# Kernel optimization log

Measured on AMD Instinct MI355X. Metric: run time of the kernel, lower is better.

Reference implementation:

```python
import jax, jax.numpy as jnp
import numpy as np

B, C, H, W = 8, 256, 32, 32
DK, HEADS = 64, 4
DQ = DK * HEADS            # lambda attention: query dim = dim_key * num_heads
DV = 256 // HEADS          # out_channels // num_heads
EPS = 1e-5
SF = DK ** (-0.25)


def setup_inputs() -> dict:
    key = jax.random.key(0)
    ks = jax.random.split(key, 6)
    inv = 1.0 / np.sqrt(C)
    return {
        "input": jax.random.normal(ks[0], (B, C, H, W), jnp.float32),
        "Wq": jax.random.normal(ks[1], (DQ, C), jnp.float32) * inv,
        "gamma_q": jnp.ones((DQ,), jnp.float32),
        "beta_q": jnp.zeros((DQ,), jnp.float32),
        "Wk": jax.random.normal(ks[2], (DK, C), jnp.float32) * inv,
        "gamma_k": jnp.ones((DK,), jnp.float32),
        "beta_k": jnp.zeros((DK,), jnp.float32),
        "Wv": jax.random.normal(ks[3], (DV, C), jnp.float32) * inv,
        "rpe": jax.random.normal(ks[4], (2 * max(H, W) - 1, 2 * max(H, W) - 1, DK), jnp.float32),
    }


def _bn(x, gamma, beta):
    # BatchNorm2d in training mode: batch stats over (B, H, W), biased variance
    mu = jnp.mean(x, axis=(0, 2, 3), keepdims=True)
    var = jnp.var(x, axis=(0, 2, 3), keepdims=True)
    xn = (x - mu) * jax.lax.rsqrt(var + EPS)
    return xn * gamma[None, :, None, None] + beta[None, :, None, None]


def reference(input, Wq, gamma_q, beta_q, Wk, gamma_k, beta_k, Wv, rpe):
    b, c, h, w = input.shape
    n = h * w
    size = max(h, w)

    # conv1x1 projections (no bias)
    q = _bn(jnp.einsum('oc,bchw->bohw', Wq, input), gamma_q, beta_q)
    k = _bn(jnp.einsum('oc,bchw->bohw', Wk, input), gamma_k, beta_k)
    v = jnp.einsum('oc,bchw->bohw', Wv, input)

    q = q.reshape(b, HEADS, DK, n) * SF          # [b,h,k,n]
    k = k.reshape(b, DK, n) * SF                 # single kv head -> [b,k,n]
    v = v.reshape(b, DV, n)                      # [b,v,n]

    # lambda attention: content lambda
    ks = jax.nn.softmax(k, axis=-1)
    context = jnp.einsum('bkn,bvn->bkv', ks, v)
    out = jnp.einsum('bkv,bhkn->bhvn', context, q)

    # positional lambda via relative position embedding gather
    pos = jnp.arange(size)
    grid = jnp.stack(jnp.meshgrid(pos, pos, indexing='ij'), axis=-1).reshape(-1, 2)  # [n,2]
    rel = grid[None, :] - grid[:, None] + (size - 1)                                 # [n,n,2]
    rg = rpe[rel[..., 0], rel[..., 1]]                                               # [n,n,k]
    pos_context = jnp.einsum('nmk,bvm->bnkv', rg, v)
    out = out + jnp.einsum('bhkn,bnkv->bhvn', q, pos_context)

    return out.reshape(b, -1, h, w)
```

## Files before the change

kernel.cpp:

```cpp
#include <hip/hip_runtime.h>

#define SFC 0.35355339059327373f

typedef __attribute__((ext_vector_type(8))) short short8;
typedef __attribute__((ext_vector_type(16))) float f32x16;
typedef unsigned short ushort_t;

__device__ __forceinline__ float4 ld4(const float* p) { return *reinterpret_cast<const float4*>(p); }
__device__ __forceinline__ void st4(float* p, float4 v) { *reinterpret_cast<float4*>(p) = v; }

union F4 { float4 v; float f[4]; };
union S8 { short8 v; ushort_t u[8]; };

__device__ __forceinline__ ushort_t bfb(float f) {
  union { float f; unsigned u; } a; a.f = f;
  unsigned r = a.u + 0x7FFFu + ((a.u >> 16) & 1u);
  return (ushort_t)(r >> 16);
}
__device__ __forceinline__ float bf2f(ushort_t u) {
  union { unsigned u; float f; } a; a.u = (unsigned)u << 16; return a.f;
}

__device__ __forceinline__ void gl16(const void* g, void* l) {
  __builtin_amdgcn_global_load_lds(
      (const __attribute__((address_space(1))) unsigned int*)g,
      (__attribute__((address_space(3))) unsigned int*)l, 16, 0, 0);
}

__global__ __launch_bounds__(256) void k_prep(
    const float* __restrict__ rpe, const float* __restrict__ wq,
    const float* __restrict__ wk, const float* __restrict__ wv,
    const float* __restrict__ x, ushort_t* __restrict__ RPEB2,
    ushort_t* __restrict__ WB, ushort_t* __restrict__ XBT)
{
  const int bx = blockIdx.x, t = threadIdx.x;
  if (bx < 63) {
    const int di = bx;
#pragma unroll
    for (int it = 0; it < 2; ++it) {
      const int slot = t + it * 256;
      const int tkc = slot >> 6;
      const int l = slot & 63, lnp = l & 31, hip = l >> 5;
      const int dj = (tkc >> 2) * 32 + lnp;
      const int k = (tkc & 3) * 16 + hip * 8;
      S8 o;
      if (dj < 63) {
        const float* s = rpe + (size_t)di * 4032 + dj * 64 + k;
        float4 a = ld4(s), b = ld4(s + 4);
        o.u[0] = bfb(a.x); o.u[1] = bfb(a.y); o.u[2] = bfb(a.z); o.u[3] = bfb(a.w);
        o.u[4] = bfb(b.x); o.u[5] = bfb(b.y); o.u[6] = bfb(b.z); o.u[7] = bfb(b.w);
      } else {
#pragma unroll
        for (int i = 0; i < 8; ++i) o.u[i] = 0;
      }
      *(short8*)(RPEB2 + (size_t)di * 4096 + tkc * 512 + l * 8) = o.v;
    }
  } else if (bx < 111) {
    const int cc = (bx - 63) * 256 + t;
    const int o = cc >> 5, k8 = (cc & 31) * 8;
    const float* src = (o < 256) ? (wq + o * 256)
                      : (o < 320) ? (wk + (o - 256) * 256)
                                  : (wv + (o - 320) * 256);
    float4 a = ld4(src + k8), b = ld4(src + k8 + 4);
    S8 s;
    s.u[0] = bfb(a.x); s.u[1] = bfb(a.y); s.u[2] = bfb(a.z); s.u[3] = bfb(a.w);
    s.u[4] = bfb(b.x); s.u[5] = bfb(b.y); s.u[6] = bfb(b.z); s.u[7] = bfb(b.w);
    *(short8*)(WB + (size_t)o * 256 + k8) = s.v;
  } else {
    const int id = (bx - 111) * 256 + t;
    const int ng = id & 8191, c8 = id >> 13;
    const int bb = ng >> 10, nn = ng & 1023;
    const float* src = x + (size_t)bb * 262144 + (size_t)(c8 * 8) * 1024 + nn;
    S8 s;
#pragma unroll
    for (int j = 0; j < 8; ++j) s.u[j] = bfb(src[(size_t)j * 1024]);
    *(short8*)(XBT + (size_t)ng * 256 + c8 * 8) = s.v;
  }
}

__global__ __launch_bounds__(256) void k_projm(
    const ushort_t* __restrict__ WB, const ushort_t* __restrict__ XBT,
    float* __restrict__ Pk, ushort_t* __restrict__ QB,
    ushort_t* __restrict__ VB2, float* __restrict__ PSUM,
    float* __restrict__ PSQ)
{
  __shared__ ushort_t At[64 * 72];
  __shared__ ushort_t Bt[128 * 72];
  const int t = threadIdx.x;
  const int bm = blockIdx.x, bn = blockIdx.y;
  const int o0 = bm * 64, col0 = bn * 128;
  const int w = t >> 6, l = t & 63, ln = l & 31, hi = l >> 5;
  const int wm = w & 1, wn = w >> 1;

  f32x16 acc0, acc1;
#pragma unroll
  for (int i = 0; i < 16; ++i) { acc0[i] = 0.f; acc1[i] = 0.f; }

  for (int k0 = 0; k0 < 256; k0 += 64) {
    __syncthreads();
#pragma unroll
    for (int i = 0; i < 2; ++i) {
      const int c = t + i * 256, row = c >> 3, k8 = (c & 7) * 8;
      *(short8*)(At + row * 72 + k8) =
          *(const short8*)(WB + (size_t)(o0 + row) * 256 + k0 + k8);
    }
#pragma unroll
    for (int i = 0; i < 4; ++i) {
      const int c = t + i * 256, row = c >> 3, k8 = (c & 7) * 8;
      *(short8*)(Bt + row * 72 + k8) =
          *(const short8*)(XBT + (size_t)(col0 + row) * 256 + k0 + k8);
    }
    __syncthreads();
    const ushort_t* ka  = At + (wm * 32 + ln) * 72 + hi * 8;
    const ushort_t* kb0 = Bt + (wn * 64 + ln) * 72 + hi * 8;
    const ushort_t* kb1 = Bt + (wn * 64 + 32 + ln) * 72 + hi * 8;
#pragma unroll
    for (int kc = 0; kc < 4; ++kc) {
      short8 a = *(const short8*)(ka + kc * 16);
      acc0 = __builtin_amdgcn_mfma_f32_32x32x16_bf16(a, *(const short8*)(kb0 + kc * 16), acc0, 0, 0, 0);
      acc1 = __builtin_amdgcn_mfma_f32_32x32x16_bf16(a, *(const short8*)(kb1 + kc * 16), acc1, 0, 0, 0);
    }
  }

  if (bm == 5) {
    const int b2 = bn >> 3;
    const int n0 = (bn & 7) * 128 + wn * 64 + ln;
#pragma unroll
    for (int r = 0; r < 16; ++r) {
      const int v = wm * 32 + (r & 3) + 8 * (r >> 2) + 4 * hi;
#pragma unroll
      for (int half = 0; half < 2; ++half) {
        const int n = n0 + half * 32;
        const int i2 = n >> 5, j2 = n & 31;
        const float val = half ? acc1[r] : acc0[r];
        VB2[(((size_t)(b2 * 32 + i2) * 2 + wm) * 2 + (j2 >> 4)) * 512
            + ((v & 31) + 32 * ((j2 >> 3) & 1)) * 8 + (j2 & 7)] = bfb(val);
      }
    }
  } else {
    if (bm == 4) {
#pragma unroll
      for (int r = 0; r < 16; ++r) {
        const int o = o0 + wm * 32 + (r & 3) + 8 * (r >> 2) + 4 * hi;
        float* dst = Pk + (size_t)(o - 256) * 8192 + col0 + wn * 64 + ln;
        dst[0]  = acc0[r];
        dst[32] = acc1[r];
      }
    } else {
      const int kcq = 2 * wm;
#pragma unroll
      for (int r = 0; r < 16; ++r) {
        const int kc = kcq + ((r >> 3) & 1);
        const int lq = ln + 32 * ((r >> 2) & 1);
        const int iq = (r & 3) + 4 * hi;
#pragma unroll
        for (int half = 0; half < 2; ++half) {
          const int n = col0 + wn * 64 + half * 32 + ln;
          const int bq_ = n >> 10, i1q = (n >> 5) & 31;
          const float val = half ? acc1[r] : acc0[r];
          QB[(((size_t)(bq_ * 32 + i1q) * 4 + bm) * 4 + kc) * 512 + lq * 8 + iq] =
              bfb(val);
        }
      }
    }
#pragma unroll
    for (int r = 0; r < 16; ++r) {
      float s1 = acc0[r] + acc1[r];
      float s2 = acc0[r] * acc0[r] + acc1[r] * acc1[r];
#pragma unroll
      for (int off = 1; off < 32; off <<= 1) {
        s1 += __shfl_xor(s1, off, 64);
        s2 += __shfl_xor(s2, off, 64);
      }
      if (ln == 0) {
        const int o = o0 + wm * 32 + (r & 3) + 8 * (r >> 2) + 4 * hi;
        PSUM[o * 128 + bn * 2 + wn] = s1;
        PSQ [o * 128 + bn * 2 + wn] = s2;
      }
    }
  }
}

__global__ __launch_bounds__(256) void k_softctx(
    const float* __restrict__ Pk, const float* __restrict__ PSUM,
    const float* __restrict__ PSQ, const float* __restrict__ gq,
    const float* __restrict__ bq, const float* __restrict__ gk,
    const float* __restrict__ bk, float* __restrict__ SCALE,
    float* __restrict__ SHIFT, const ushort_t* __restrict__ VB2,
    ushort_t* __restrict__ CTXB)
{
  __shared__ float red[8];
  __shared__ float scsh[2];
  __shared__ float cpart[4][64];
  const int t = threadIdx.x;

  if (blockIdx.x >= 512) {
    const int ch = blockIdx.x - 512;
    float s1 = 0.f, s2 = 0.f;
    if (t < 128) { s1 = PSUM[ch * 128 + t]; s2 = PSQ[ch * 128 + t]; }
#pragma unroll
    for (int off = 1; off < 64; off <<= 1) {
      s1 += __shfl_xor(s1, off, 64);
      s2 += __shfl_xor(s2, off, 64);
    }
    if ((t & 63) == 0) { red[t >> 6] = s1; red[4 + (t >> 6)] = s2; }
    __syncthreads();
    if (t == 0) {
      s1 = red[0] + red[1] + red[2] + red[3];
      s2 = red[4] + red[5] + red[6] + red[7];
      const float mu = s1 * (1.0f / 8192.0f);
      const float var = s2 * (1.0f / 8192.0f) - mu * mu;
      const float sc = rsqrtf(var + 1e-5f) * gq[ch] * SFC;
      SCALE[ch] = sc;
      SHIFT[ch] = bq[ch] * SFC - mu * sc;
    }
    return;
  }

  const int b = blockIdx.x >> 6, kc = blockIdx.x & 63;
  {
    const int ch = 256 + kc;
    float s1 = 0.f, s2 = 0.f;
    if (t < 128) { s1 = PSUM[ch * 128 + t]; s2 = PSQ[ch * 128 + t]; }
#pragma unroll
    for (int off = 1; off < 64; off <<= 1) {
      s1 += __shfl_xor(s1, off, 64);
      s2 += __shfl_xor(s2, off, 64);
    }
    if ((t & 63) == 0) { red[t >> 6] = s1; red[4 + (t >> 6)] = s2; }
    __syncthreads();
    if (t == 0) {
      s1 = red[0] + red[1] + red[2] + red[3];
      s2 = red[4] + red[5] + red[6] + red[7];
      const float mu = s1 * (1.0f / 8192.0f);
      const float var = s2 * (1.0f / 8192.0f) - mu * mu;
      const float sc = rsqrtf(var + 1e-5f) * gk[kc] * SFC;
      scsh[0] = sc;
      scsh[1] = bk[kc] * SFC - mu * sc;
    }
    __syncthreads();
  }
  const float sc = scsh[0], sh = scsh[1];

  const float4* rowp = (const float4*)(Pk + (size_t)kc * 8192 + b * 1024);
  float4 pv = rowp[t];
  float y0 = pv.x * sc + sh, y1 = pv.y * sc + sh;
  float y2 = pv.z * sc + sh, y3 = pv.w * sc + sh;
  float m = fmaxf(fmaxf(y0, y1), fmaxf(y2, y3));
#pragma unroll
  for (int off = 32; off; off >>= 1) m = fmaxf(m, __shfl_xor(m, off, 64));
  __shared__ float red2[8];
  const int w = t >> 6, l = t & 63;
  if (l == 0) red2[w] = m;
  __syncthreads();
  m = fmaxf(fmaxf(red2[0], red2[1]), fmaxf(red2[2], red2[3]));
  const float e0 = __expf(y0 - m), e1 = __expf(y1 - m);
  const float e2 = __expf(y2 - m), e3 = __expf(y3 - m);
  float su = e0 + e1 + e2 + e3;
#pragma unroll
  for (int off = 32; off; off >>= 1) su += __shfl_xor(su, off, 64);
  if (l == 0) red2[4 + w] = su;
  __syncthreads();
  const float inv = 1.0f / (red2[4] + red2[5] + red2[6] + red2[7]);
  const float k0v = e0 * inv, k1v = e1 * inv, k2v = e2 * inv, k3v = e3 * inv;

  const int n0 = t * 4;
  const int i2 = n0 >> 5;
  const int cX = (n0 >> 4) & 1, hi2 = (n0 >> 3) & 1, i0 = n0 & 7;
  const ushort_t* vbL = VB2 + (((size_t)(b * 32 + i2) * 2 + 0) * 2 + cX) * 512
                        + (32 * hi2) * 8 + i0;
  const ushort_t* vbH = vbL + 1024;
  float a64[64];
#pragma unroll
  for (int v = 0; v < 32; ++v) {
    ushort4 u = *(const ushort4*)(vbL + v * 8);
    a64[v] = k0v * bf2f(u.x) + k1v * bf2f(u.y) + k2v * bf2f(u.z) + k3v * bf2f(u.w);
  }
#pragma unroll
  for (int v = 0; v < 32; ++v) {
    ushort4 u = *(const ushort4*)(vbH + v * 8);
    a64[32 + v] = k0v * bf2f(u.x) + k1v * bf2f(u.y) + k2v * bf2f(u.z) + k3v * bf2f(u.w);
  }
  float c32[32];
#pragma unroll
  for (int j = 0; j < 32; ++j) {
    const float mine = (l & 32) ? a64[j + 32] : a64[j];
    const float send = (l & 32) ? a64[j] : a64[j + 32];
    c32[j] = mine + __shfl_xor(send, 32, 64);
  }
  float c16[16];
#pragma unroll
  for (int j = 0; j < 16; ++j) {
    const float mine = (l & 16) ? c32[j + 16] : c32[j];
    const float send = (l & 16) ? c32[j] : c32[j + 16];
    c16[j] = mine + __shfl_xor(send, 16, 64);
  }
  float c8[8];
#pragma unroll
  for (int j = 0; j < 8; ++j) {
    const float mine = (l & 8) ? c16[j + 8] : c16[j];
    const float send = (l & 8) ? c16[j] : c16[j + 8];
    c8[j] = mine + __shfl_xor(send, 8, 64);
  }
  float c4[4];
#pragma unroll
  for (int j = 0; j < 4; ++j) {
    const float mine = (l & 4) ? c8[j + 4] : c8[j];
    const float send = (l & 4) ? c8[j] : c8[j + 4];
    c4[j] = mine + __shfl_xor(send, 4, 64);
  }
  float c2[2];
#pragma unroll
  for (int j = 0; j < 2; ++j) {
    const float mine = (l & 2) ? c4[j + 2] : c4[j];
    const float send = (l & 2) ? c4[j] : c4[j + 2];
    c2[j] = mine + __shfl_xor(send, 2, 64);
  }
  {
    const float mine = (l & 1) ? c2[1] : c2[0];
    const float send = (l & 1) ? c2[0] : c2[1];
    cpart[w][l] = mine + __shfl_xor(send, 1, 64);
  }
  __syncthreads();
  if (w == 0) {
    const float s = cpart[0][l] + cpart[1][l] + cpart[2][l] + cpart[3][l];
    CTXB[(size_t)b * 4608 + l * 72 + kc] = bfb(s);
  }
}

extern __shared__ char ldsc[];

__global__ __launch_bounds__(512) void k_pos(
    const ushort_t* __restrict__ QB, const ushort_t* __restrict__ RPEB2,
    const ushort_t* __restrict__ VB2, const float* __restrict__ SCALE,
    const float* __restrict__ SHIFT, const ushort_t* __restrict__ CTXB,
    float* __restrict__ out)
{
  float* out_l = (float*)ldsc;
  ushort_t* SlB = (ushort_t*)(ldsc + 33792);
  char* CtxL = ldsc + 54272;

  const int t = threadIdx.x;
  const int b = blockIdx.x >> 5, i1 = blockIdx.x & 31;
  const int w = t >> 6, l = t & 63, ln = l & 31, hi = l >> 5;
  const int m = w & 3, g = w >> 2;

  {
    const char* cs = (const char*)CTXB + (size_t)b * 9216;
    gl16(cs + w * 1024 + l * 16, CtxL + w * 1024 + l * 16);
    if (w == 0) gl16(cs + 8192 + l * 16, CtxL + 8192 + l * 16);
  }

  const ushort_t* rbase = RPEB2 + (size_t)(g * 16 - i1 + 31) * 4096;
  const ushort_t* vbase = VB2 + (size_t)(b * 32 + g * 16) * 2048;

  short8 rA[8], rB[8];
#pragma unroll
  for (int f = 0; f < 8; ++f) rA[f] = *(const short8*)(rbase + f * 512 + l * 8);

  short8 qf[4];
  {
    const ushort_t* qb = QB + (((size_t)(b * 32 + i1) * 4 + m) * 4) * 512 + l * 8;
#pragma unroll
    for (int kc = 0; kc < 4; ++kc) {
      S8 raw; raw.v = *(const short8*)(qb + kc * 512);
      const int chb = m * 64 + kc * 16 + hi * 8;
      F4 s0, s1, h0, h1;
      s0.v = ld4(SCALE + chb); s1.v = ld4(SCALE + chb + 4);
      h0.v = ld4(SHIFT + chb); h1.v = ld4(SHIFT + chb + 4);
      S8 o;
#pragma unroll
      for (int i = 0; i < 8; ++i) {
        const float f = bf2f(raw.u[i]);
        const float scv = (i < 4) ? s0.f[i] : s1.f[i - 4];
        const float shv = (i < 4) ? h0.f[i] : h1.f[i - 4];
        o.u[i] = bfb(f * scv + shv);
      }
      qf[kc] = o.v;
    }
  }

  f32x16 sv0, sv1;
#pragma unroll
  for (int i = 0; i < 16; ++i) { sv0[i] = 0.f; sv1[i] = 0.f; }

  ushort_t* sm = SlB + w * 1280;

  auto body = [&](int s, const short8* R) {
    const ushort_t* vp = vbase + (size_t)s * 2048 + l * 8;
    short8 v00 = *(const short8*)(vp);
    short8 v01 = *(const short8*)(vp + 512);
    short8 v10 = *(const short8*)(vp + 1024);
    short8 v11 = *(const short8*)(vp + 1536);
    f32x16 t0, t1;
#pragma unroll
    for (int i = 0; i < 16; ++i) { t0[i] = 0.f; t1[i] = 0.f; }
#pragma unroll
    for (int kc = 0; kc < 4; ++kc) {
      t0 = __builtin_amdgcn_mfma_f32_32x32x16_bf16(qf[kc], R[kc],     t0, 0, 0, 0);
      t1 = __builtin_amdgcn_mfma_f32_32x32x16_bf16(qf[kc], R[4 + kc], t1, 0, 0, 0);
    }
#pragma unroll
    for (int r = 0; r < 16; ++r) {
      const int j1 = (r & 3) + 8 * (r >> 2) + 4 * hi;
      const int j2a = ln + j1 - 31;
      const int j2b = 32 + ln + j1 - 31;
      if ((unsigned)j2a < 32u) sm[j1 * 40 + j2a] = bfb(t0[r]);
      if ((unsigned)j2b < 32u) sm[j1 * 40 + j2b] = bfb(t1[r]);
    }
    const ushort_t* sa = sm + ln * 40 + hi * 8;
    short8 sA0 = *(const short8*)(sa);
    short8 sA1 = *(const short8*)(sa + 16);
    sv0 = __builtin_amdgcn_mfma_f32_32x32x16_bf16(sA0, v00, sv0, 0, 0, 0);
    sv0 = __builtin_amdgcn_mfma_f32_32x32x16_bf16(sA1, v01, sv0, 0, 0, 0);
    sv1 = __builtin_amdgcn_mfma_f32_32x32x16_bf16(sA0, v10, sv1, 0, 0, 0);
    sv1 = __builtin_amdgcn_mfma_f32_32x32x16_bf16(sA1, v11, sv1, 0, 0, 0);
  };

  for (int s = 0; s < 16; s += 2) {
    {
      const ushort_t* rn = rbase + (size_t)(s + 1) * 4096;
#pragma unroll
      for (int f = 0; f < 8; ++f) rB[f] = *(const short8*)(rn + f * 512 + l * 8);
    }
    body(s, rA);
    if (s + 2 < 16) {
      const ushort_t* rn = rbase + (size_t)(s + 2) * 4096;
#pragma unroll
      for (int f = 0; f < 8; ++f) rA[f] = *(const short8*)(rn + f * 512 + l * 8);
    }
    body(s + 1, rB);
  }

  __syncthreads();

  if (g == 0) {
    const ushort_t* cb = (const ushort_t*)CtxL;
    const ushort_t* c0 = cb + ln * 72 + hi * 8;
    const ushort_t* c1 = cb + (32 + ln) * 72 + hi * 8;
#pragma unroll
    for (int kc = 0; kc < 4; ++kc) {
      sv0 = __builtin_amdgcn_mfma_f32_32x32x16_bf16(qf[kc], *(const short8*)(c0 + kc * 16), sv0, 0, 0, 0);
      sv1 = __builtin_amdgcn_mfma_f32_32x32x16_bf16(qf[kc], *(const short8*)(c1 + kc * 16), sv1, 0, 0, 0);
    }
  } else {
#pragma unroll
    for (int r = 0; r < 16; ++r) {
      const int j1 = (r & 3) + 8 * (r >> 2) + 4 * hi;
      out_l[(m * 64 + ln) * 33 + j1]      = sv0[r];
      out_l[(m * 64 + 32 + ln) * 33 + j1] = sv1[r];
    }
  }
  __syncthreads();
  if (g == 0) {
#pragma unroll
    for (int r = 0; r < 16; ++r) {
      const int j1 = (r & 3) + 8 * (r >> 2) + 4 * hi;
      out_l[(m * 64 + ln) * 33 + j1]      += sv0[r];
      out_l[(m * 64 + 32 + ln) * 33 + j1] += sv1[r];
    }
  }
  __syncthreads();
  {
    const int ch = t >> 1, jh = (t & 1) * 16;
    float* dst = out + (size_t)b * 262144 + (size_t)ch * 1024 + i1 * 32 + jh;
    const float* srow = out_l + ch * 33 + jh;
#pragma unroll
    for (int gq2 = 0; gq2 < 4; ++gq2)
      st4(dst + gq2 * 4, make_float4(srow[gq2 * 4], srow[gq2 * 4 + 1],
                                     srow[gq2 * 4 + 2], srow[gq2 * 4 + 3]));
  }
}

extern "C" void kernel_launch(void* const* d_in, const int* in_sizes, int n_in,
                              void* d_out, int out_size, void* d_ws, size_t ws_size,
                              hipStream_t stream) {
  const float* x   = (const float*)d_in[0];
  const float* wq  = (const float*)d_in[1];
  const float* gq  = (const float*)d_in[2];
  const float* bq  = (const float*)d_in[3];
  const float* wk  = (const float*)d_in[4];
  const float* gk  = (const float*)d_in[5];
  const float* bk  = (const float*)d_in[6];
  const float* wv  = (const float*)d_in[7];
  const float* rpe = (const float*)d_in[8];
  float* out = (float*)d_out;
  char* W = (char*)d_ws;

  float* Pk       = (float*)W;
  ushort_t* QB    = (ushort_t*)(W + 2097152);
  float* PSUM     = (float*)(W + 6291456);
  float* PSQ      = (float*)(W + 6455296);
  float* SCALE    = (float*)(W + 6619136);
  float* SHIFT    = (float*)(W + 6621184);
  ushort_t* CTXB  = (ushort_t*)(W + 6623232);
  ushort_t* RPEB2 = (ushort_t*)(W + 6696960);
  ushort_t* VB2   = (ushort_t*)(W + 7213056);
  ushort_t* WB    = (ushort_t*)(W + 8261632);
  ushort_t* XBT   = (ushort_t*)(W + 8458240);

  k_prep<<<1135, 256, 0, stream>>>(rpe, wq, wk, wv, x, RPEB2, WB, XBT);
  k_projm<<<dim3(6, 64), 256, 0, stream>>>(WB, XBT, Pk, QB, VB2, PSUM, PSQ);
  k_softctx<<<768, 256, 0, stream>>>(Pk, PSUM, PSQ, gq, bq, gk, bk,
                                     SCALE, SHIFT, VB2, CTXB);

  hipFuncSetAttribute((const void*)k_pos,
                      hipFuncAttributeMaxDynamicSharedMemorySize, 63488);
  k_pos<<<256, 512, 63488, stream>>>(QB, RPEB2, VB2, SCALE, SHIFT, CTXB, out);
}
```

Measured before the change: 59.69 us.

## Stage projection outputs through LDS and split k_pos waves by head pairs

```diff
diff --git a/kernel.cpp b/kernel.cpp
--- a/kernel.cpp
+++ b/kernel.cpp
@@ -84,8 +84,9 @@
     ushort_t* __restrict__ VB2, float* __restrict__ PSUM,
     float* __restrict__ PSQ)
 {
-  __shared__ ushort_t At[64 * 72];
-  __shared__ ushort_t Bt[128 * 72];
+  __shared__ ushort_t SM[13824];
+  ushort_t* At = SM;
+  ushort_t* Bt = SM + 4608;
   const int t = threadIdx.x;
   const int bm = blockIdx.x, bn = blockIdx.y;
   const int o0 = bm * 64, col0 = bn * 128;
@@ -123,30 +124,74 @@
   }
 
   if (bm == 5) {
-    const int b2 = bn >> 3;
-    const int n0 = (bn & 7) * 128 + wn * 64 + ln;
+    __syncthreads();
+    {
+      const int n0l = wn * 64 + ln;
+#pragma unroll
+      for (int r = 0; r < 16; ++r) {
+        const int v = wm * 32 + (r & 3) + 8 * (r >> 2) + 4 * hi;
+#pragma unroll
+        for (int half = 0; half < 2; ++half) {
+          const int nl = n0l + half * 32;
+          const int i2l = nl >> 5, j2 = nl & 31;
+          const float val = half ? acc1[r] : acc0[r];
+          SM[((i2l * 4 + wm * 2 + (j2 >> 4)) << 9)
+             + ((v & 31) + 32 * ((j2 >> 3) & 1)) * 8 + (j2 & 7)] = bfb(val);
+        }
+      }
+    }
+    __syncthreads();
+    {
+      const int b2 = bn >> 3, i2b0 = (bn & 7) * 4;
+      const int slot = t >> 4, off = (t & 15) * 32;
+      const int i2l = slot >> 2, sub = slot & 3;
+      ushort_t* gdst = VB2 + ((size_t)((b2 * 32 + i2b0 + i2l) * 4 + sub)) * 512 + off;
+      const ushort_t* lsrc = SM + slot * 512 + off;
+#pragma unroll
+      for (int c = 0; c < 4; ++c)
+        *(short8*)(gdst + c * 8) = *(const short8*)(lsrc + c * 8);
+    }
+  } else if (bm == 4) {
 #pragma unroll
     for (int r = 0; r < 16; ++r) {
-      const int v = wm * 32 + (r & 3) + 8 * (r >> 2) + 4 * hi;
-#pragma unroll
-      for (int half = 0; half < 2; ++half) {
-        const int n = n0 + half * 32;
-        const int i2 = n >> 5, j2 = n & 31;
-        const float val = half ? acc1[r] : acc0[r];
-        VB2[(((size_t)(b2 * 32 + i2) * 2 + wm) * 2 + (j2 >> 4)) * 512
-            + ((v & 31) + 32 * ((j2 >> 3) & 1)) * 8 + (j2 & 7)] = bfb(val);
+      const int o = o0 + wm * 32 + (r & 3) + 8 * (r >> 2) + 4 * hi;
+      float* dst = Pk + (size_t)(o - 256) * 8192 + col0 + wn * 64 + ln;
+      dst[0]  = acc0[r];
+      dst[32] = acc1[r];
+    }
+#pragma unroll
+    for (int r = 0; r < 16; ++r) {
+      float s1 = acc0[r] + acc1[r];
+      float s2 = acc0[r] * acc0[r] + acc1[r] * acc1[r];
+#pragma unroll
+      for (int off = 1; off < 32; off <<= 1) {
+        s1 += __shfl_xor(s1, off, 64);
+        s2 += __shfl_xor(s2, off, 64);
+      }
+      if (ln == 0) {
+        const int o = o0 + wm * 32 + (r & 3) + 8 * (r >> 2) + 4 * hi;
+        PSUM[o * 128 + bn * 2 + wn] = s1;
+        PSQ [o * 128 + bn * 2 + wn] = s2;
       }
     }
   } else {
-    if (bm == 4) {
-#pragma unroll
-      for (int r = 0; r < 16; ++r) {
+#pragma unroll
+    for (int r = 0; r < 16; ++r) {
+      float s1 = acc0[r] + acc1[r];
+      float s2 = acc0[r] * acc0[r] + acc1[r] * acc1[r];
+#pragma unroll
+      for (int off = 1; off < 32; off <<= 1) {
+        s1 += __shfl_xor(s1, off, 64);
+        s2 += __shfl_xor(s2, off, 64);
+      }
+      if (ln == 0) {
         const int o = o0 + wm * 32 + (r & 3) + 8 * (r >> 2) + 4 * hi;
-        float* dst = Pk + (size_t)(o - 256) * 8192 + col0 + wn * 64 + ln;
-        dst[0]  = acc0[r];
-        dst[32] = acc1[r];
-      }
-    } else {
+        PSUM[o * 128 + bn * 2 + wn] = s1;
+        PSQ [o * 128 + bn * 2 + wn] = s2;
+      }
+    }
+    __syncthreads();
+    {
       const int kcq = 2 * wm;
 #pragma unroll
       for (int r = 0; r < 16; ++r) {
@@ -155,28 +200,22 @@
         const int iq = (r & 3) + 4 * hi;
 #pragma unroll
         for (int half = 0; half < 2; ++half) {
-          const int n = col0 + wn * 64 + half * 32 + ln;
-          const int bq_ = n >> 10, i1q = (n >> 5) & 31;
+          const int i1l = wn * 2 + half;
           const float val = half ? acc1[r] : acc0[r];
-          QB[(((size_t)(bq_ * 32 + i1q) * 4 + bm) * 4 + kc) * 512 + lq * 8 + iq] =
-              bfb(val);
+          SM[((i1l * 4 + kc) << 9) + lq * 8 + iq] = bfb(val);
         }
       }
     }
-#pragma unroll
-    for (int r = 0; r < 16; ++r) {
-      float s1 = acc0[r] + acc1[r];
-      float s2 = acc0[r] * acc0[r] + acc1[r] * acc1[r];
-#pragma unroll
-      for (int off = 1; off < 32; off <<= 1) {
-        s1 += __shfl_xor(s1, off, 64);
-        s2 += __shfl_xor(s2, off, 64);
-      }
-      if (ln == 0) {
-        const int o = o0 + wm * 32 + (r & 3) + 8 * (r >> 2) + 4 * hi;
-        PSUM[o * 128 + bn * 2 + wn] = s1;
-        PSQ [o * 128 + bn * 2 + wn] = s2;
-      }
+    __syncthreads();
+    {
+      const int b0 = col0 >> 10, i1b = (col0 >> 5) & 31;
+      const int slot = t >> 4, off = (t & 15) * 32;
+      const int i1l = slot >> 2, kc2 = slot & 3;
+      ushort_t* gdst = QB + (((size_t)(b0 * 32 + i1b + i1l) * 4 + bm) * 4 + kc2) * 512 + off;
+      const ushort_t* lsrc = SM + slot * 512 + off;
+#pragma unroll
+      for (int c = 0; c < 4; ++c)
+        *(short8*)(gdst + c * 8) = *(const short8*)(lsrc + c * 8);
     }
   }
 }
@@ -338,12 +377,13 @@
 {
   float* out_l = (float*)ldsc;
   ushort_t* SlB = (ushort_t*)(ldsc + 33792);
-  char* CtxL = ldsc + 54272;
+  char* CtxL = ldsc + 74752;
 
   const int t = threadIdx.x;
   const int b = blockIdx.x >> 5, i1 = blockIdx.x & 31;
   const int w = t >> 6, l = t & 63, ln = l & 31, hi = l >> 5;
-  const int m = w & 3, g = w >> 2;
+  const int hp = w & 1, g = w >> 1;
+  const int m0 = hp * 2, m1 = m0 + 1;
 
   {
     const char* cs = (const char*)CTXB + (size_t)b * 9216;
@@ -351,40 +391,81 @@
     if (w == 0) gl16(cs + 8192 + l * 16, CtxL + 8192 + l * 16);
   }
 
-  const ushort_t* rbase = RPEB2 + (size_t)(g * 16 - i1 + 31) * 4096;
-  const ushort_t* vbase = VB2 + (size_t)(b * 32 + g * 16) * 2048;
+  const ushort_t* rbase = RPEB2 + (size_t)(g * 8 - i1 + 31) * 4096;
+  const ushort_t* vbase = VB2 + (size_t)(b * 32 + g * 8) * 2048;
 
   short8 rA[8], rB[8];
 #pragma unroll
   for (int f = 0; f < 8; ++f) rA[f] = *(const short8*)(rbase + f * 512 + l * 8);
 
-  short8 qf[4];
+  short8 qf0[4], qf1[4];
   {
-    const ushort_t* qb = QB + (((size_t)(b * 32 + i1) * 4 + m) * 4) * 512 + l * 8;
-#pragma unroll
-    for (int kc = 0; kc < 4; ++kc) {
-      S8 raw; raw.v = *(const short8*)(qb + kc * 512);
-      const int chb = m * 64 + kc * 16 + hi * 8;
-      F4 s0, s1, h0, h1;
-      s0.v = ld4(SCALE + chb); s1.v = ld4(SCALE + chb + 4);
-      h0.v = ld4(SHIFT + chb); h1.v = ld4(SHIFT + chb + 4);
-      S8 o;
-#pragma unroll
-      for (int i = 0; i < 8; ++i) {
-        const float f = bf2f(raw.u[i]);
-        const float scv = (i < 4) ? s0.f[i] : s1.f[i - 4];
-        const float shv = (i < 4) ? h0.f[i] : h1.f[i - 4];
-        o.u[i] = bfb(f * scv + shv);
-      }
-      qf[kc] = o.v;
-    }
-  }
-
-  f32x16 sv0, sv1;
-#pragma unroll
-  for (int i = 0; i < 16; ++i) { sv0[i] = 0.f; sv1[i] = 0.f; }
-
-  ushort_t* sm = SlB + w * 1280;
+    const ushort_t* qb0 = QB + (((size_t)(b * 32 + i1) * 4 + m0) * 4) * 512 + l * 8;
+#pragma unroll
+    for (int hh = 0; hh < 2; ++hh) {
+      const ushort_t* qb = qb0 + (size_t)hh * 4 * 512;
+      const int mh = m0 + hh;
+#pragma unroll
+      for (int kc = 0; kc < 4; ++kc) {
+        S8 raw; raw.v = *(const short8*)(qb + kc * 512);
+        const int chb = mh * 64 + kc * 16 + hi * 8;
+        F4 s0, s1, h0, h1;
+        s0.v = ld4(SCALE + chb); s1.v = ld4(SCALE + chb + 4);
+        h0.v = ld4(SHIFT + chb); h1.v = ld4(SHIFT + chb + 4);
+        S8 o;
+#pragma unroll
+        for (int i = 0; i < 8; ++i) {
+          const float f = bf2f(raw.u[i]);
+          const float scv = (i < 4) ? s0.f[i] : s1.f[i - 4];
+          const float shv = (i < 4) ? h0.f[i] : h1.f[i - 4];
+          o.u[i] = bfb(f * scv + shv);
+        }
+        if (hh == 0) qf0[kc] = o.v; else qf1[kc] = o.v;
+      }
+    }
+  }
+
+  f32x16 s00, s01, s10, s11;
+#pragma unroll
+  for (int i = 0; i < 16; ++i) { s00[i] = 0.f; s01[i] = 0.f; s10[i] = 0.f; s11[i] = 0.f; }
+
+  ushort_t* sm0 = SlB + w * 2560;
+  ushort_t* sm1 = sm0 + 1280;
+
+  auto headTSV = [&](const short8* R, const short8* qf, ushort_t* smh,
+                     short8 v00, short8 v01, short8 v10, short8 v11,
+                     f32x16& sA, f32x16& sB) {
+    f32x16 tt;
+#pragma unroll
+    for (int i = 0; i < 16; ++i) tt[i] = 0.f;
+#pragma unroll
+    for (int kc = 0; kc < 4; ++kc)
+      tt = __builtin_amdgcn_mfma_f32_32x32x16_bf16(qf[kc], R[kc], tt, 0, 0, 0);
+#pragma unroll
+    for (int r = 0; r < 16; ++r) {
+      const int j1 = (r & 3) + 8 * (r >> 2) + 4 * hi;
+      const int j2 = ln + j1 - 31;
+      if ((unsigned)j2 < 32u) smh[j1 * 40 + j2] = bfb(tt[r]);
+    }
+#pragma unroll
+    for (int i = 0; i < 16; ++i) tt[i] = 0.f;
+#pragma unroll
+    for (int kc = 0; kc < 4; ++kc)
+      tt = __builtin_amdgcn_mfma_f32_32x32x16_bf16(qf[kc], R[4 + kc], tt, 0, 0, 0);
+#pragma unroll
+    for (int r = 0; r < 16; ++r) {
+      const int j1 = (r & 3) + 8 * (r >> 2) + 4 * hi;
+      const int j2 = 32 + ln + j1 - 31;
+      if ((unsigned)j2 < 32u) smh[j1 * 40 + j2] = bfb(tt[r]);
+    }
+    const ushort_t* sa = smh + ln * 40 + hi * 8;
+    short8 sA0 = *(const short8*)(sa);
+    short8 sA1 = *(const short8*)(sa + 16);
+    sA = __builtin_amdgcn_mfma_f32_32x32x16_bf16(sA0, v00, sA, 0, 0, 0);
+    sA = __builtin_amdgcn_mfma_f32_32x32x16_bf16(sA1, v01, sA, 0, 0, 0);
+    sB = __builtin_amdgcn_mfma_f32_32x32x16_bf16(sA0, v10, sB, 0, 0, 0);
+    sB = __builtin_amdgcn_mfma_f32_32x32x16_bf16(sA1, v11, sB, 0, 0, 0);
+  };
 
   auto body = [&](int s, const short8* R) {
     const ushort_t* vp = vbase + (size_t)s * 2048 + l * 8;
@@ -392,39 +473,18 @@
     short8 v01 = *(const short8*)(vp + 512);
     short8 v10 = *(const short8*)(vp + 1024);
     short8 v11 = *(const short8*)(vp + 1536);
-    f32x16 t0, t1;
-#pragma unroll
-    for (int i = 0; i < 16; ++i) { t0[i] = 0.f; t1[i] = 0.f; }
-#pragma unroll
-    for (int kc = 0; kc < 4; ++kc) {
-      t0 = __builtin_amdgcn_mfma_f32_32x32x16_bf16(qf[kc], R[kc],     t0, 0, 0, 0);
-      t1 = __builtin_amdgcn_mfma_f32_32x32x16_bf16(qf[kc], R[4 + kc], t1, 0, 0, 0);
-    }
-#pragma unroll
-    for (int r = 0; r < 16; ++r) {
-      const int j1 = (r & 3) + 8 * (r >> 2) + 4 * hi;
-      const int j2a = ln + j1 - 31;
-      const int j2b = 32 + ln + j1 - 31;
-      if ((unsigned)j2a < 32u) sm[j1 * 40 + j2a] = bfb(t0[r]);
-      if ((unsigned)j2b < 32u) sm[j1 * 40 + j2b] = bfb(t1[r]);
-    }
-    const ushort_t* sa = sm + ln * 40 + hi * 8;
-    short8 sA0 = *(const short8*)(sa);
-    short8 sA1 = *(const short8*)(sa + 16);
-    sv0 = __builtin_amdgcn_mfma_f32_32x32x16_bf16(sA0, v00, sv0, 0, 0, 0);
-    sv0 = __builtin_amdgcn_mfma_f32_32x32x16_bf16(sA1, v01, sv0, 0, 0, 0);
-    sv1 = __builtin_amdgcn_mfma_f32_32x32x16_bf16(sA0, v10, sv1, 0, 0, 0);
-    sv1 = __builtin_amdgcn_mfma_f32_32x32x16_bf16(sA1, v11, sv1, 0, 0, 0);
+    headTSV(R, qf0, sm0, v00, v01, v10, v11, s00, s01);
+    headTSV(R, qf1, sm1, v00, v01, v10, v11, s10, s11);
   };
 
-  for (int s = 0; s < 16; s += 2) {
+  for (int s = 0; s < 8; s += 2) {
     {
       const ushort_t* rn = rbase + (size_t)(s + 1) * 4096;
 #pragma unroll
       for (int f = 0; f < 8; ++f) rB[f] = *(const short8*)(rn + f * 512 + l * 8);
     }
     body(s, rA);
-    if (s + 2 < 16) {
+    if (s + 2 < 8) {
       const ushort_t* rn = rbase + (size_t)(s + 2) * 4096;
 #pragma unroll
       for (int f = 0; f < 8; ++f) rA[f] = *(const short8*)(rn + f * 512 + l * 8);
@@ -440,26 +500,35 @@
     const ushort_t* c1 = cb + (32 + ln) * 72 + hi * 8;
 #pragma unroll
     for (int kc = 0; kc < 4; ++kc) {
-      sv0 = __builtin_amdgcn_mfma_f32_32x32x16_bf16(qf[kc], *(const short8*)(c0 + kc * 16), sv0, 0, 0, 0);
-      sv1 = __builtin_amdgcn_mfma_f32_32x32x16_bf16(qf[kc], *(const short8*)(c1 + kc * 16), sv1, 0, 0, 0);
-    }
-  } else {
+      short8 f0 = *(const short8*)(c0 + kc * 16);
+      short8 f1 = *(const short8*)(c1 + kc * 16);
+      s00 = __builtin_amdgcn_mfma_f32_32x32x16_bf16(qf0[kc], f0, s00, 0, 0, 0);
+      s01 = __builtin_amdgcn_mfma_f32_32x32x16_bf16(qf0[kc], f1, s01, 0, 0, 0);
+      s10 = __builtin_amdgcn_mfma_f32_32x32x16_bf16(qf1[kc], f0, s10, 0, 0, 0);
+      s11 = __builtin_amdgcn_mfma_f32_32x32x16_bf16(qf1[kc], f1, s11, 0, 0, 0);
+    }
+  }
+
+  auto emit = [&](const f32x16& acc, int mm, int tau, bool add) {
 #pragma unroll
     for (int r = 0; r < 16; ++r) {
       const int j1 = (r & 3) + 8 * (r >> 2) + 4 * hi;
-      out_l[(m * 64 + ln) * 33 + j1]      = sv0[r];
-      out_l[(m * 64 + 32 + ln) * 33 + j1] = sv1[r];
-    }
-  }
-  __syncthreads();
-  if (g == 0) {
-#pragma unroll
-    for (int r = 0; r < 16; ++r) {
-      const int j1 = (r & 3) + 8 * (r >> 2) + 4 * hi;
-      out_l[(m * 64 + ln) * 33 + j1]      += sv0[r];
-      out_l[(m * 64 + 32 + ln) * 33 + j1] += sv1[r];
-    }
-  }
+      float* p = &out_l[(mm * 64 + tau * 32 + ln) * 33 + j1];
+      if (add) *p += acc[r]; else *p = acc[r];
+    }
+  };
+  auto emit4 = [&](bool add) {
+    emit(s00, m0, 0, add); emit(s01, m0, 1, add);
+    emit(s10, m1, 0, add); emit(s11, m1, 1, add);
+  };
+
+  if (g == 3) emit4(false);
+  __syncthreads();
+  if (g == 2) emit4(true);
+  __syncthreads();
+  if (g == 1) emit4(true);
+  __syncthreads();
+  if (g == 0) emit4(true);
   __syncthreads();
   {
     const int ch = t >> 1, jh = (t & 1) * 16;
@@ -505,6 +574,6 @@
                                      SCALE, SHIFT, VB2, CTXB);
 
   hipFuncSetAttribute((const void*)k_pos,
-                      hipFuncAttributeMaxDynamicSharedMemorySize, 63488);
-  k_pos<<<256, 512, 63488, stream>>>(QB, RPEB2, VB2, SCALE, SHIFT, CTXB, out);
-}
+                      hipFuncAttributeMaxDynamicSharedMemorySize, 83968);
+  k_pos<<<256, 512, 83968, stream>>>(QB, RPEB2, VB2, SCALE, SHIFT, CTXB, out);
+}
```

Result: slower. 62.47 us (+4.7%).
